# Optimization experiments

Measured on AMD Instinct MI355X. Metric: run time of the kernel, lower is better.

The kernel has to match this reference:

```python
import jax, jax.numpy as jnp
import numpy as np

DIM = 256
HEADS = 8


def _ln(x, g, b, eps=1e-5):
    mu = jnp.mean(x, axis=-1, keepdims=True)
    var = jnp.var(x, axis=-1, keepdims=True)
    return (x - mu) * jax.lax.rsqrt(var + eps) * g + b


def setup_inputs() -> dict:
    key = jax.random.key(0)
    ks = jax.random.split(key, 12)
    d = DIM
    s = lambda fan: 1.0 / np.sqrt(fan)
    return {
        "x": jax.random.normal(ks[0], (1, d, 64, 64), dtype=jnp.float32),
        "ln1_g": jnp.ones((d,), jnp.float32),
        "ln1_b": jnp.zeros((d,), jnp.float32),
        "w_qkv": jax.random.normal(ks[1], (3 * d, d), jnp.float32) * s(d),
        "b_qkv": jnp.zeros((3 * d,), jnp.float32),
        "w_proj": jax.random.normal(ks[2], (d, d), jnp.float32) * s(d),
        "b_proj": jnp.zeros((d,), jnp.float32),
        "ln2_g": jnp.ones((d,), jnp.float32),
        "ln2_b": jnp.zeros((d,), jnp.float32),
        "w_mlp1": jax.random.normal(ks[3], (4 * d, d), jnp.float32) * s(d),
        "b_mlp1": jnp.zeros((4 * d,), jnp.float32),
        "w_mlp2": jax.random.normal(ks[4], (d, 4 * d), jnp.float32) * s(4 * d),
        "b_mlp2": jnp.zeros((d,), jnp.float32),
    }


def reference(x, ln1_g, ln1_b, w_qkv, b_qkv, w_proj, b_proj,
              ln2_g, ln2_b, w_mlp1, b_mlp1, w_mlp2, b_mlp2):
    B, C, H, W = x.shape
    hd = HEADS
    d = C // hd
    scale = d ** (-0.5)
    # work channels-last: [B, H, W, C] -> [B, HW, C]
    xl = jnp.transpose(x, (0, 2, 3, 1)).reshape(B, H * W, C)

    # --- attention branch ---
    xn = _ln(xl, ln1_g, ln1_b)
    qkv = jnp.einsum('bnc,oc->bno', xn, w_qkv) + b_qkv  # [B, N, 3C]
    q, k, v = jnp.split(qkv, 3, axis=-1)
    def heads(t):  # [B,N,C] -> [B,h,N,d]
        return jnp.transpose(t.reshape(B, H * W, hd, d), (0, 2, 1, 3))
    q, k, v = heads(q), heads(k), heads(v)
    attn = jax.nn.softmax(jnp.einsum('bhnd,bhmd->bhnm', q, k) * scale, axis=-1)
    out = jnp.einsum('bhnm,bhmd->bhnd', attn, v)  # [B,h,N,d]
    out = jnp.transpose(out, (0, 2, 1, 3)).reshape(B, H * W, C)
    xl = xl + jnp.einsum('bnc,oc->bno', out, w_proj) + b_proj

    # --- MLP branch ---
    xn = _ln(xl, ln2_g, ln2_b)
    h1 = jax.nn.gelu(jnp.einsum('bnc,oc->bno', xn, w_mlp1) + b_mlp1,
                     approximate=False)
    xl = xl + jnp.einsum('bnf,of->bno', h1, w_mlp2) + b_mlp2

    return jnp.transpose(xl.reshape(B, H, W, C), (0, 3, 1, 2))
```

## Files before the change

### kernel.cpp

```cpp
#include <hip/hip_runtime.h>
#include <hip/hip_bf16.h>

typedef __bf16 bf16_t;
typedef __bf16 bf16x8 __attribute__((ext_vector_type(8)));
typedef __bf16 bf16x4 __attribute__((ext_vector_type(4)));
typedef float  f32x4  __attribute__((ext_vector_type(4)));
typedef unsigned int uint;
typedef uint u32x4 __attribute__((ext_vector_type(4)));

#define MFMA(a,b,c) __builtin_amdgcn_mfma_f32_16x16x32_bf16((a),(b),(c),0,0,0)
#define SPLIT 4

__device__ __forceinline__ size_t pidx(int n, int k, int K) {
  return (size_t)(n >> 4) * (K << 4) + ((k >> 3) << 7) + ((n & 15) << 3) + (k & 7);
}

__device__ __forceinline__ uint packbf2(float lo, float hi) {
  unsigned short a = __builtin_bit_cast(unsigned short, (bf16_t)lo);
  unsigned short b = __builtin_bit_cast(unsigned short, (bf16_t)hi);
  return (uint)a | ((uint)b << 16);
}

__global__ __launch_bounds__(256) void prep(const float* __restrict__ w_qkv,
                                            const float* __restrict__ w_proj,
                                            const float* __restrict__ w_mlp1,
                                            const float* __restrict__ w_mlp2,
                                            bf16_t* __restrict__ wq, bf16_t* __restrict__ wp,
                                            bf16_t* __restrict__ w1, bf16_t* __restrict__ w2,
                                            const float* __restrict__ x,
                                            const float* __restrict__ g,
                                            const float* __restrict__ bta,
                                            float* __restrict__ xl,
                                            bf16_t* __restrict__ xn) {
  __shared__ float tile[256][33];
  __shared__ float psum[8][32], psq[8][32], mu_s[32], rs_s[32];
  int b = blockIdx.x;
  if (b < 384) {
    const float* src; bf16_t* dst; int t0, ksh;
    if (b < 96)       { src = w_qkv;  dst = wq; ksh = 5; t0 = b * 256; }
    else if (b < 128) { src = w_proj; dst = wp; ksh = 5; t0 = (b - 96) * 256; }
    else if (b < 256) { src = w_mlp1; dst = w1; ksh = 5; t0 = (b - 128) * 256; }
    else              { src = w_mlp2; dst = w2; ksh = 7; t0 = (b - 256) * 256; }
    int t = t0 + threadIdx.x;
    int n = t >> ksh, kb = t & ((1 << ksh) - 1);
    int K = 8 << ksh;
    const float* p = src + (size_t)n * K + kb * 8;
    float4 a = *(const float4*)p;
    float4 c = *(const float4*)(p + 4);
    bf16x8 o = {(bf16_t)a.x, (bf16_t)a.y, (bf16_t)a.z, (bf16_t)a.w,
                (bf16_t)c.x, (bf16_t)c.y, (bf16_t)c.z, (bf16_t)c.w};
    *(bf16x8*)(dst + (size_t)(n >> 4) * (K << 4) + kb * 128 + ((n & 15) << 3)) = o;
    return;
  }
  int t = threadIdx.x, n0 = (b - 384) * 32;
  int lane32 = t & 31, grp = t >> 5;
#pragma unroll
  for (int it = 0; it < 32; ++it) {
    int c = grp + it * 8;
    tile[c][lane32] = x[(size_t)c * 4096 + n0 + lane32];
  }
  __syncthreads();
  float s = 0.f, sq = 0.f;
#pragma unroll
  for (int ci = 0; ci < 32; ++ci) {
    float v = tile[grp * 32 + ci][lane32];
    s += v; sq += v * v;
  }
  psum[grp][lane32] = s; psq[grp][lane32] = sq;
  __syncthreads();
  if (t < 32) {
    float S = 0.f, Q = 0.f;
#pragma unroll
    for (int p = 0; p < 8; ++p) { S += psum[p][t]; Q += psq[p][t]; }
    float mu = S * (1.0f / 256.0f);
    float var = Q * (1.0f / 256.0f) - mu * mu;
    mu_s[t] = mu; rs_s[t] = rsqrtf(var + 1e-5f);
  }
  __syncthreads();
  {
    float mu = mu_s[lane32], rs = rs_s[lane32];
    int row = n0 + lane32;
    bf16_t* op = xn + (size_t)(row >> 4) * 4096 + ((row & 15) << 3);
#pragma unroll
    for (int cc8 = 0; cc8 < 4; ++cc8) {
      int c0 = grp * 32 + cc8 * 8;
      bf16x8 o;
#pragma unroll
      for (int j = 0; j < 8; ++j) {
        int c = c0 + j;
        o[j] = (bf16_t)((tile[c][lane32] - mu) * rs * g[c] + bta[c]);
      }
      *(bf16x8*)(op + ((c0 >> 3) << 7)) = o;
    }
  }
#pragma unroll
  for (int it = 0; it < 4; ++it) {
    int j = grp + it * 8;
#pragma unroll
    for (int c0 = 0; c0 < 256; c0 += 32)
      xl[(size_t)(n0 + j) * 256 + c0 + lane32] = tile[c0 + lane32][j];
  }
}

template <int K, int EPI, int RPW, int KS = 1>
__global__ __launch_bounds__(256) void gemm_bt(const bf16_t* __restrict__ A,
                                               const bf16_t* __restrict__ W,
                                               const float* __restrict__ bias,
                                               void* __restrict__ outp, int ldn,
                                               const float* __restrict__ resid,
                                               const float* __restrict__ g2,
                                               const float* __restrict__ bt2,
                                               bf16_t* __restrict__ xn2p) {
  constexpr int RB = RPW / 16;
  constexpr int KLEN = K / KS;
  int w = threadIdx.x >> 6, lane = threadIdx.x & 63;
  int quad = lane >> 4, idx = lane & 15;
  int row0, col0;
  if constexpr (EPI == 6) { row0 = blockIdx.x * 16; col0 = w * 64; }
  else { row0 = blockIdx.x * (4 * RPW) + w * RPW; col0 = blockIdx.y * 64; }
  int kb0 = (KS > 1) ? blockIdx.z * KLEN : 0;
  f32x4 acc[RB][4];
#pragma unroll
  for (int rb = 0; rb < RB; ++rb)
#pragma unroll
    for (int nb = 0; nb < 4; ++nb) acc[rb][nb] = (f32x4){0.f, 0.f, 0.f, 0.f};
  const bf16_t* abase = A + (size_t)(row0 >> 4) * (K << 4) + quad * 128 + idx * 8;
  const bf16_t* wbase = W + (size_t)(col0 >> 4) * (K << 4) + quad * 128 + idx * 8;
#pragma unroll 4
  for (int k0 = kb0; k0 < kb0 + KLEN; k0 += 32) {
    bf16x8 a[RB];
#pragma unroll
    for (int rb = 0; rb < RB; ++rb)
      a[rb] = *(const bf16x8*)(abase + (size_t)rb * (K << 4) + k0 * 16);
#pragma unroll
    for (int nb = 0; nb < 4; ++nb) {
      bf16x8 b = *(const bf16x8*)(wbase + (size_t)nb * (K << 4) + k0 * 16);
#pragma unroll
      for (int rb = 0; rb < RB; ++rb) acc[rb][nb] = MFMA(a[rb], b, acc[rb][nb]);
    }
  }

  if constexpr (EPI == 6) {
    __shared__ float lns[4][2][16];
    __shared__ bf16_t tile[16][256];
    float vv[4][4];
    float ps[4] = {0.f, 0.f, 0.f, 0.f}, pq[4] = {0.f, 0.f, 0.f, 0.f};
#pragma unroll
    for (int nb = 0; nb < 4; ++nb) {
      int c = col0 + nb * 16 + idx;
      float bv = bias[c];
#pragma unroll
      for (int r = 0; r < 4; ++r) {
        int rr = row0 + quad * 4 + r;
        float t = acc[0][nb][r] + bv + resid[(size_t)rr * 256 + c];
        vv[nb][r] = t;
        ((float*)outp)[(size_t)rr * 256 + c] = t;
        ps[r] += t; pq[r] += t * t;
      }
    }
#pragma unroll
    for (int m = 1; m < 16; m <<= 1)
#pragma unroll
      for (int r = 0; r < 4; ++r) {
        ps[r] += __shfl_xor(ps[r], m);
        pq[r] += __shfl_xor(pq[r], m);
      }
    if (idx == 0)
#pragma unroll
      for (int r = 0; r < 4; ++r) {
        lns[w][0][quad * 4 + r] = ps[r];
        lns[w][1][quad * 4 + r] = pq[r];
      }
    __syncthreads();
    float mu[4], rs[4];
#pragma unroll
    for (int r = 0; r < 4; ++r) {
      int row = quad * 4 + r;
      float S = (lns[0][0][row] + lns[1][0][row]) + (lns[2][0][row] + lns[3][0][row]);
      float Q = (lns[0][1][row] + lns[1][1][row]) + (lns[2][1][row] + lns[3][1][row]);
      float m_ = S * (1.0f / 256.0f);
      mu[r] = m_;
      rs[r] = rsqrtf(Q * (1.0f / 256.0f) - m_ * m_ + 1e-5f);
    }
#pragma unroll
    for (int nb = 0; nb < 4; ++nb) {
      int c = col0 + nb * 16 + idx;
      float gg = g2[c], bb = bt2[c];
#pragma unroll
      for (int r = 0; r < 4; ++r)
        tile[quad * 4 + r][c] = (bf16_t)((vv[nb][r] - mu[r]) * rs[r] * gg + bb);
    }
    __syncthreads();
    {
      int t = threadIdx.x;
      int row = t >> 4, k0 = (t & 15) * 16;
      int grr = row0 + row;
      bf16_t* op = xn2p + (size_t)(grr >> 4) * 4096 + ((grr & 15) << 3);
      *(bf16x8*)(op + ((k0 >> 3) << 7)) = *(const bf16x8*)&tile[row][k0];
      *(bf16x8*)(op + (((k0 + 8) >> 3) << 7)) = *(const bf16x8*)&tile[row][k0 + 8];
    }
    return;
  }

#pragma unroll
  for (int nb = 0; nb < 4; ++nb) {
    int c = col0 + nb * 16 + idx;
    float bv = (EPI == 4) ? 0.f : bias[c];
    if constexpr (EPI == 5) {
      int n = row0 + quad * 4;
      f32x4 o;
#pragma unroll
      for (int r = 0; r < 4; ++r)
        o[r] = acc[0][nb][r] + bv + resid[(size_t)(n + r) * 256 + c];
      *(f32x4*)((float*)outp + (size_t)c * 4096 + n) = o;
    } else {
#pragma unroll
      for (int rb = 0; rb < RB; ++rb)
#pragma unroll
        for (int r = 0; r < 4; ++r) {
          int rr = row0 + rb * 16 + quad * 4 + r;
          float v = acc[rb][nb][r] + bv;
          if constexpr (EPI == 1) {
            float z = v * (0.7978845608f + 0.0356774081f * v * v);
            float t = __builtin_amdgcn_exp2f(z * 2.885390082f);
            float th = 1.f - 2.f * __builtin_amdgcn_rcpf(t + 1.f);
            v = 0.5f * v * (1.f + th);
            ((bf16_t*)outp)[pidx(rr, c, ldn)] = (bf16_t)v;
          } else if constexpr (EPI == 4) {
            ((float*)outp)[((size_t)blockIdx.z * 4096 + rr) * ldn + c] = v;
          } else {
            bf16_t* qh = (bf16_t*)outp;
            bf16_t* kh = qh + 1048576;
            bf16_t* vp = kh + 1048576;
            if (c < 256) {
              qh[(size_t)(c >> 5) * 131072 + rr * 32 + (c & 31)] = (bf16_t)v;
            } else if (c < 512) {
              kh[(size_t)((c - 256) >> 5) * 131072 + rr * 32 + (c & 31)] = (bf16_t)v;
            } else {
              vp[(size_t)((c - 512) >> 5) * 131072 + (rr >> 5) * 1024 + (c & 31) * 32 + (rr & 31)] = (bf16_t)v;
            }
          }
        }
    }
  }
}

__device__ __forceinline__ void quad_transpose(const uint p[4][2], bf16x8& lo, bf16x8& hi) {
  auto sA0 = __builtin_amdgcn_permlane32_swap((int)p[0][0], (int)p[1][0], false, false);
  auto sA1 = __builtin_amdgcn_permlane32_swap((int)p[0][1], (int)p[1][1], false, false);
  auto sB0 = __builtin_amdgcn_permlane16_swap(sA0[0], sA0[1], false, false);
  auto sB1 = __builtin_amdgcn_permlane16_swap(sA1[0], sA1[1], false, false);
  u32x4 w0 = {(uint)sB0[0], (uint)sB1[0], (uint)sB0[1], (uint)sB1[1]};
  lo = __builtin_bit_cast(bf16x8, w0);
  auto tA0 = __builtin_amdgcn_permlane32_swap((int)p[2][0], (int)p[3][0], false, false);
  auto tA1 = __builtin_amdgcn_permlane32_swap((int)p[2][1], (int)p[3][1], false, false);
  auto tB0 = __builtin_amdgcn_permlane16_swap(tA0[0], tA0[1], false, false);
  auto tB1 = __builtin_amdgcn_permlane16_swap(tA1[0], tA1[1], false, false);
  u32x4 w1 = {(uint)tB0[0], (uint)tB1[0], (uint)tB0[1], (uint)tB1[1]};
  hi = __builtin_bit_cast(bf16x8, w1);
}

__global__ __launch_bounds__(256, 4) void attn_split(const bf16_t* __restrict__ qkvh,
                                                     uint* __restrict__ o_part,
                                                     float* __restrict__ l_part) {
  int w = threadIdx.x >> 6, lane = threadIdx.x & 63;
  int quad = lane >> 4, idx = lane & 15;
  int h  = blockIdx.x & 7;
  int qt = (blockIdx.x >> 3) & 31;
  int sp = blockIdx.x >> 8;
  int qrow = qt * 128 + w * 32;
  const bf16_t* qh = qkvh + (size_t)h * 131072;
  const bf16_t* kh = qh + 8 * 131072;
  const bf16_t* vp = kh + 8 * 131072;
  const float cs = 0.25503518f;
  bf16x8 qr0 = *(const bf16x8*)(qh + (size_t)(qrow + idx) * 32 + quad * 8);
  bf16x8 qr1 = *(const bf16x8*)(qh + (size_t)(qrow + 16 + idx) * 32 + quad * 8);
  bf16x8 qf0, qf1, ones1;
#pragma unroll
  for (int j = 0; j < 8; ++j) {
    qf0[j] = (bf16_t)((float)qr0[j] * cs);
    qf1[j] = (bf16_t)((float)qr1[j] * cs);
    ones1[j] = (bf16_t)1.0f;
  }
  f32x4 o00 = {0.f,0.f,0.f,0.f}, o01 = {0.f,0.f,0.f,0.f};
  f32x4 o10 = {0.f,0.f,0.f,0.f}, o11 = {0.f,0.f,0.f,0.f};
  f32x4 lsA = {0.f,0.f,0.f,0.f}, lsB = {0.f,0.f,0.f,0.f};
  const f32x4 zero = {0.f,0.f,0.f,0.f};
  int kbase = sp * 1024;

  bf16x8 kf[4];
#pragma unroll
  for (int kb = 0; kb < 4; ++kb)
    kf[kb] = *(const bf16x8*)(kh + (size_t)(kbase + kb * 16 + idx) * 32 + quad * 8);

  for (int kt = 0; kt < 16; ++kt) {
    int k0 = kbase + kt * 64;
    int k1 = kbase + ((kt + 1) & 15) * 64;
    const bf16_t* vt = vp + (size_t)(k0 >> 5) * 1024 + quad * 8;
    bf16x8 vv0 = *(const bf16x8*)(vt + idx * 32);
    bf16x8 vv1 = *(const bf16x8*)(vt + (idx + 16) * 32);
    bf16x8 vv2 = *(const bf16x8*)(vt + 1024 + idx * 32);
    bf16x8 vv3 = *(const bf16x8*)(vt + 1024 + (idx + 16) * 32);
    bf16x8 kfn[4];
#pragma unroll
    for (int kb = 0; kb < 4; ++kb)
      kfn[kb] = *(const bf16x8*)(kh + (size_t)(k1 + kb * 16 + idx) * 32 + quad * 8);
    __builtin_amdgcn_s_setprio(1);
    uint p0[4][2], p1[4][2];
#pragma unroll
    for (int kb = 0; kb < 4; ++kb) {
      f32x4 s0 = MFMA(kf[kb], qf0, zero);
      f32x4 s1 = MFMA(kf[kb], qf1, zero);
      float a0 = __builtin_amdgcn_exp2f(s0[0]), a1 = __builtin_amdgcn_exp2f(s0[1]);
      float a2 = __builtin_amdgcn_exp2f(s0[2]), a3 = __builtin_amdgcn_exp2f(s0[3]);
      float b0 = __builtin_amdgcn_exp2f(s1[0]), b1 = __builtin_amdgcn_exp2f(s1[1]);
      float b2 = __builtin_amdgcn_exp2f(s1[2]), b3 = __builtin_amdgcn_exp2f(s1[3]);
      p0[kb][0] = packbf2(a0, a1); p0[kb][1] = packbf2(a2, a3);
      p1[kb][0] = packbf2(b0, b1); p1[kb][1] = packbf2(b2, b3);
    }
    bf16x8 pa0, pa1, pb0, pb1;
    quad_transpose(p0, pa0, pa1);
    quad_transpose(p1, pb0, pb1);
    o00 = MFMA(pa0, vv0, o00);
    o01 = MFMA(pa0, vv1, o01);
    o10 = MFMA(pb0, vv0, o10);
    o11 = MFMA(pb0, vv1, o11);
    lsA = MFMA(pa0, ones1, lsA);
    lsB = MFMA(pb0, ones1, lsB);
    o00 = MFMA(pa1, vv2, o00);
    o01 = MFMA(pa1, vv3, o01);
    o10 = MFMA(pb1, vv2, o10);
    o11 = MFMA(pb1, vv3, o11);
    lsA = MFMA(pa1, ones1, lsA);
    lsB = MFMA(pb1, ones1, lsB);
    __builtin_amdgcn_s_setprio(0);
#pragma unroll
    for (int kb = 0; kb < 4; ++kb) kf[kb] = kfn[kb];
  }
  if (idx == 0) {
    float* lp = l_part + ((size_t)sp * 8 + h) * 4096 + qrow;
#pragma unroll
    for (int r = 0; r < 4; ++r) {
      lp[quad * 4 + r]      = lsA[r];
      lp[16 + quad * 4 + r] = lsB[r];
    }
  }
#pragma unroll
  for (int r = 0; r < 4; ++r) {
    int n0 = qrow + quad * 4 + r;
    o_part[(((size_t)sp * 4096 + n0) * 8 + h) * 16 + idx] = packbf2(o00[r], o01[r]);
    int n1 = n0 + 16;
    o_part[(((size_t)sp * 4096 + n1) * 8 + h) * 16 + idx] = packbf2(o10[r], o11[r]);
  }
}

__global__ __launch_bounds__(256) void attn_norm(const uint* __restrict__ o_part,
                                                 const float* __restrict__ l_part,
                                                 bf16_t* __restrict__ attn) {
  int t = blockIdx.x * 256 + threadIdx.x;
  int j0 = (t & 3) * 4;
  int h  = (t >> 2) & 7;
  int n  = t >> 5;
  float l = 0.f;
#pragma unroll
  for (int s = 0; s < SPLIT; ++s) l += l_part[((size_t)s * 8 + h) * 4096 + n];
  float inv = 1.0f / l;
  float alo[4] = {0.f,0.f,0.f,0.f}, ahi[4] = {0.f,0.f,0.f,0.f};
#pragma unroll
  for (int s = 0; s < SPLIT; ++s) {
    const uint* p = o_part + (((size_t)s * 4096 + n) * 8 + h) * 16 + j0;
    uint4 v = *(const uint4*)p;
    uint vv[4] = {v.x, v.y, v.z, v.w};
#pragma unroll
    for (int jj = 0; jj < 4; ++jj) {
      alo[jj] += __builtin_bit_cast(float, vv[jj] << 16);
      ahi[jj] += __builtin_bit_cast(float, vv[jj] & 0xffff0000u);
    }
  }
  bf16x4 lo = {(bf16_t)(alo[0] * inv), (bf16_t)(alo[1] * inv),
               (bf16_t)(alo[2] * inv), (bf16_t)(alo[3] * inv)};
  bf16x4 hi = {(bf16_t)(ahi[0] * inv), (bf16_t)(ahi[1] * inv),
               (bf16_t)(ahi[2] * inv), (bf16_t)(ahi[3] * inv)};
  int k1 = h * 32 + j0;
  int k2 = k1 + 16;
  *(bf16x4*)(attn + (size_t)(n >> 4) * 4096 + ((k1 >> 3) << 7) + ((n & 15) << 3) + (k1 & 7)) = lo;
  *(bf16x4*)(attn + (size_t)(n >> 4) * 4096 + ((k2 >> 3) << 7) + ((n & 15) << 3) + (k2 & 7)) = hi;
}

extern "C" void kernel_launch(void* const* d_in, const int* in_sizes, int n_in,
                              void* d_out, int out_size, void* d_ws, size_t ws_size,
                              hipStream_t stream) {
  const float* x      = (const float*)d_in[0];
  const float* ln1_g  = (const float*)d_in[1];
  const float* ln1_b  = (const float*)d_in[2];
  const float* w_qkv  = (const float*)d_in[3];
  const float* b_qkv  = (const float*)d_in[4];
  const float* w_proj = (const float*)d_in[5];
  const float* b_proj = (const float*)d_in[6];
  const float* ln2_g  = (const float*)d_in[7];
  const float* ln2_b  = (const float*)d_in[8];
  const float* w_mlp1 = (const float*)d_in[9];
  const float* b_mlp1 = (const float*)d_in[10];
  const float* w_mlp2 = (const float*)d_in[11];
  const float* b_mlp2 = (const float*)d_in[12];

  char* ws = (char*)d_ws;
  bf16_t* qkvh   = (bf16_t*)(ws + 0);
  float*  xl     = (float*)(ws + (6u << 20));
  bf16_t* xn     = (bf16_t*)(ws + (10u << 20));
  uint*   o_part = (uint*)(ws + (12u << 20));
  bf16_t* attn   = (bf16_t*)(ws + (20u << 20));
  float*  xl2    = (float*)(ws + (10u << 20));
  bf16_t* xn2    = (bf16_t*)(ws + (14u << 20));
  bf16_t* h1     = (bf16_t*)(ws + 0);
  bf16_t* wq     = (bf16_t*)(ws + (32u << 20));
  bf16_t* wp     = wq + 196608;
  bf16_t* w1     = wp + 65536;
  bf16_t* w2     = w1 + 262144;
  float*  l_part = (float*)(ws + (34304u << 10));

  prep<<<512, 256, 0, stream>>>(w_qkv, w_proj, w_mlp1, w_mlp2, wq, wp, w1, w2,
                                x, ln1_g, ln1_b, xl, xn);

  gemm_bt<256, 3, 16><<<dim3(64, 12), 256, 0, stream>>>(
      xn, wq, b_qkv, qkvh, 768, nullptr, nullptr, nullptr, nullptr);
  attn_split<<<256 * SPLIT, 256, 0, stream>>>(qkvh, o_part, l_part);
  attn_norm<<<512, 256, 0, stream>>>(o_part, l_part, attn);

  gemm_bt<256, 6, 16, 1><<<256, 256, 0, stream>>>(
      attn, wp, b_proj, xl2, 256, xl, ln2_g, ln2_b, xn2);

  gemm_bt<256, 1, 16><<<dim3(64, 16), 256, 0, stream>>>(
      xn2, w1, b_mlp1, h1, 1024, nullptr, nullptr, nullptr, nullptr);
  gemm_bt<1024, 5, 16, 1><<<dim3(64, 4), 256, 0, stream>>>(
      h1, w2, b_mlp2, d_out, 256, xl2, nullptr, nullptr, nullptr);
}
```

Measured before the change: 163.8 us.

## Software-pipeline attention loop: compute next tile's P while doing current PV MFMAs

Restructures the split-K attention inner loop into a two-stage software pipeline with ping-pong K fragment buffers. The QK^T MFMAs, exp2 and transposes for tile t+1 are issued in the same block as the PV MFMAs for tile t, so the exp and transpose work can overlap with matrix work. K loads are prefetched two tiles ahead. This raises register pressure from the doubled K and P buffers, and the wrap-around loads on the last iterations fetch tiles that are never used.

```diff
diff --git a/kernel.cpp b/kernel.cpp
--- a/kernel.cpp
+++ b/kernel.cpp
@@ -287,30 +287,15 @@
   f32x4 lsA = {0.f,0.f,0.f,0.f}, lsB = {0.f,0.f,0.f,0.f};
   const f32x4 zero = {0.f,0.f,0.f,0.f};
   int kbase = sp * 1024;
-
-  bf16x8 kf[4];
-#pragma unroll
-  for (int kb = 0; kb < 4; ++kb)
-    kf[kb] = *(const bf16x8*)(kh + (size_t)(kbase + kb * 16 + idx) * 32 + quad * 8);
-
-  for (int kt = 0; kt < 16; ++kt) {
-    int k0 = kbase + kt * 64;
-    int k1 = kbase + ((kt + 1) & 15) * 64;
-    const bf16_t* vt = vp + (size_t)(k0 >> 5) * 1024 + quad * 8;
-    bf16x8 vv0 = *(const bf16x8*)(vt + idx * 32);
-    bf16x8 vv1 = *(const bf16x8*)(vt + (idx + 16) * 32);
-    bf16x8 vv2 = *(const bf16x8*)(vt + 1024 + idx * 32);
-    bf16x8 vv3 = *(const bf16x8*)(vt + 1024 + (idx + 16) * 32);
-    bf16x8 kfn[4];
-#pragma unroll
-    for (int kb = 0; kb < 4; ++kb)
-      kfn[kb] = *(const bf16x8*)(kh + (size_t)(k1 + kb * 16 + idx) * 32 + quad * 8);
-    __builtin_amdgcn_s_setprio(1);
+  const bf16_t* kfbase = kh + (size_t)idx * 32 + quad * 8;
+
+  auto make_p = [&](const bf16x8 (&kfx)[4], bf16x8& oaL, bf16x8& oaH,
+                    bf16x8& obL, bf16x8& obH) {
     uint p0[4][2], p1[4][2];
 #pragma unroll
     for (int kb = 0; kb < 4; ++kb) {
-      f32x4 s0 = MFMA(kf[kb], qf0, zero);
-      f32x4 s1 = MFMA(kf[kb], qf1, zero);
+      f32x4 s0 = MFMA(kfx[kb], qf0, zero);
+      f32x4 s1 = MFMA(kfx[kb], qf1, zero);
       float a0 = __builtin_amdgcn_exp2f(s0[0]), a1 = __builtin_amdgcn_exp2f(s0[1]);
       float a2 = __builtin_amdgcn_exp2f(s0[2]), a3 = __builtin_amdgcn_exp2f(s0[3]);
       float b0 = __builtin_amdgcn_exp2f(s1[0]), b1 = __builtin_amdgcn_exp2f(s1[1]);
@@ -318,24 +303,66 @@
       p0[kb][0] = packbf2(a0, a1); p0[kb][1] = packbf2(a2, a3);
       p1[kb][0] = packbf2(b0, b1); p1[kb][1] = packbf2(b2, b3);
     }
-    bf16x8 pa0, pa1, pb0, pb1;
-    quad_transpose(p0, pa0, pa1);
-    quad_transpose(p1, pb0, pb1);
-    o00 = MFMA(pa0, vv0, o00);
-    o01 = MFMA(pa0, vv1, o01);
-    o10 = MFMA(pb0, vv0, o10);
-    o11 = MFMA(pb0, vv1, o11);
-    lsA = MFMA(pa0, ones1, lsA);
-    lsB = MFMA(pb0, ones1, lsB);
-    o00 = MFMA(pa1, vv2, o00);
-    o01 = MFMA(pa1, vv3, o01);
-    o10 = MFMA(pb1, vv2, o10);
-    o11 = MFMA(pb1, vv3, o11);
-    lsA = MFMA(pa1, ones1, lsA);
-    lsB = MFMA(pb1, ones1, lsB);
-    __builtin_amdgcn_s_setprio(0);
-#pragma unroll
-    for (int kb = 0; kb < 4; ++kb) kf[kb] = kfn[kb];
+    quad_transpose(p0, oaL, oaH);
+    quad_transpose(p1, obL, obH);
+  };
+
+  bf16x8 kfA[4], kfB[4];
+#pragma unroll
+  for (int kb = 0; kb < 4; ++kb)
+    kfA[kb] = *(const bf16x8*)(kfbase + (size_t)(kbase + kb * 16) * 32);
+#pragma unroll
+  for (int kb = 0; kb < 4; ++kb)
+    kfB[kb] = *(const bf16x8*)(kfbase + (size_t)(kbase + 64 + kb * 16) * 32);
+
+  bf16x8 AaL, AaH, AbL, AbH;
+  bf16x8 BaL, BaH, BbL, BbH;
+  make_p(kfA, AaL, AaH, AbL, AbH);
+
+  for (int t = 0; t < 8; ++t) {
+    int kt0 = 2 * t;
+    {
+      int k0 = kbase + kt0 * 64;
+      const bf16_t* vt = vp + (size_t)(k0 >> 5) * 1024 + quad * 8;
+      bf16x8 vv0 = *(const bf16x8*)(vt + idx * 32);
+      bf16x8 vv1 = *(const bf16x8*)(vt + (idx + 16) * 32);
+      bf16x8 vv2 = *(const bf16x8*)(vt + 1024 + idx * 32);
+      bf16x8 vv3 = *(const bf16x8*)(vt + 1024 + (idx + 16) * 32);
+      int kn = kbase + ((kt0 + 2) & 15) * 64;
+#pragma unroll
+      for (int kb = 0; kb < 4; ++kb)
+        kfA[kb] = *(const bf16x8*)(kfbase + (size_t)(kn + kb * 16) * 32);
+      __builtin_amdgcn_s_setprio(1);
+      make_p(kfB, BaL, BaH, BbL, BbH);
+      o00 = MFMA(AaL, vv0, o00); o01 = MFMA(AaL, vv1, o01);
+      o10 = MFMA(AbL, vv0, o10); o11 = MFMA(AbL, vv1, o11);
+      lsA = MFMA(AaL, ones1, lsA); lsB = MFMA(AbL, ones1, lsB);
+      o00 = MFMA(AaH, vv2, o00); o01 = MFMA(AaH, vv3, o01);
+      o10 = MFMA(AbH, vv2, o10); o11 = MFMA(AbH, vv3, o11);
+      lsA = MFMA(AaH, ones1, lsA); lsB = MFMA(AbH, ones1, lsB);
+      __builtin_amdgcn_s_setprio(0);
+    }
+    {
+      int k0 = kbase + (kt0 + 1) * 64;
+      const bf16_t* vt = vp + (size_t)(k0 >> 5) * 1024 + quad * 8;
+      bf16x8 vv0 = *(const bf16x8*)(vt + idx * 32);
+      bf16x8 vv1 = *(const bf16x8*)(vt + (idx + 16) * 32);
+      bf16x8 vv2 = *(const bf16x8*)(vt + 1024 + idx * 32);
+      bf16x8 vv3 = *(const bf16x8*)(vt + 1024 + (idx + 16) * 32);
+      int kn = kbase + ((kt0 + 3) & 15) * 64;
+#pragma unroll
+      for (int kb = 0; kb < 4; ++kb)
+        kfB[kb] = *(const bf16x8*)(kfbase + (size_t)(kn + kb * 16) * 32);
+      __builtin_amdgcn_s_setprio(1);
+      make_p(kfA, AaL, AaH, AbL, AbH);
+      o00 = MFMA(BaL, vv0, o00); o01 = MFMA(BaL, vv1, o01);
+      o10 = MFMA(BbL, vv0, o10); o11 = MFMA(BbL, vv1, o11);
+      lsA = MFMA(BaL, ones1, lsA); lsB = MFMA(BbL, ones1, lsB);
+      o00 = MFMA(BaH, vv2, o00); o01 = MFMA(BaH, vv3, o01);
+      o10 = MFMA(BbH, vv2, o10); o11 = MFMA(BbH, vv3, o11);
+      lsA = MFMA(BaH, ones1, lsA); lsB = MFMA(BbH, ones1, lsB);
+      __builtin_amdgcn_s_setprio(0);
+    }
   }
   if (idx == 0) {
     float* lp = l_part + ((size_t)sp * 8 + h) * 4096 + qrow;
```

After: 173.1 us. 5.6% more time.

## Fuse split-K attention reduction into attention kernel via shared memory

Applied to the files above, without the earlier changes.

Each block now covers 32 query rows of one head, and its four waves each handle a different quarter of the keys instead of separate blocks per split. The partial outputs and row sums are combined in shared memory and normalised in the same kernel, which removes the attn_norm launch and the global round trip of bf16 partials. In exchange, every wave of a block now reads a different range of K/V, so K/V reuse across waves within a block is lost, and a block barrier plus extra LDS traffic is added. The partials also stay in fp32 rather than being rounded to bf16 before the reduction.

```diff
diff --git a/kernel.cpp b/kernel.cpp
--- a/kernel.cpp
+++ b/kernel.cpp
@@ -9,7 +9,6 @@
 typedef uint u32x4 __attribute__((ext_vector_type(4)));
 
 #define MFMA(a,b,c) __builtin_amdgcn_mfma_f32_16x16x32_bf16((a),(b),(c),0,0,0)
-#define SPLIT 4
 
 __device__ __forceinline__ size_t pidx(int n, int k, int K) {
   return (size_t)(n >> 4) * (K << 4) + ((k >> 3) << 7) + ((n & 15) << 3) + (k & 7);
@@ -260,15 +259,15 @@
   hi = __builtin_bit_cast(bf16x8, w1);
 }
 
-__global__ __launch_bounds__(256, 4) void attn_split(const bf16_t* __restrict__ qkvh,
-                                                     uint* __restrict__ o_part,
-                                                     float* __restrict__ l_part) {
+__global__ __launch_bounds__(256, 4) void attn_fused(const bf16_t* __restrict__ qkvh,
+                                                     bf16_t* __restrict__ attn) {
+  __shared__ float sO[4][32][33];
+  __shared__ float sL[4][32];
   int w = threadIdx.x >> 6, lane = threadIdx.x & 63;
   int quad = lane >> 4, idx = lane & 15;
   int h  = blockIdx.x & 7;
-  int qt = (blockIdx.x >> 3) & 31;
-  int sp = blockIdx.x >> 8;
-  int qrow = qt * 128 + w * 32;
+  int qt = blockIdx.x >> 3;
+  int qrow = qt * 32;
   const bf16_t* qh = qkvh + (size_t)h * 131072;
   const bf16_t* kh = qh + 8 * 131072;
   const bf16_t* vp = kh + 8 * 131072;
@@ -286,7 +285,7 @@
   f32x4 o10 = {0.f,0.f,0.f,0.f}, o11 = {0.f,0.f,0.f,0.f};
   f32x4 lsA = {0.f,0.f,0.f,0.f}, lsB = {0.f,0.f,0.f,0.f};
   const f32x4 zero = {0.f,0.f,0.f,0.f};
-  int kbase = sp * 1024;
+  int kbase = w * 1024;
 
   bf16x8 kf[4];
 #pragma unroll
@@ -337,54 +336,40 @@
 #pragma unroll
     for (int kb = 0; kb < 4; ++kb) kf[kb] = kfn[kb];
   }
+#pragma unroll
+  for (int r = 0; r < 4; ++r) {
+    int rl = quad * 4 + r;
+    sO[w][rl][idx]           = o00[r];
+    sO[w][rl][idx + 16]      = o01[r];
+    sO[w][16 + rl][idx]      = o10[r];
+    sO[w][16 + rl][idx + 16] = o11[r];
+  }
   if (idx == 0) {
-    float* lp = l_part + ((size_t)sp * 8 + h) * 4096 + qrow;
 #pragma unroll
     for (int r = 0; r < 4; ++r) {
-      lp[quad * 4 + r]      = lsA[r];
-      lp[16 + quad * 4 + r] = lsB[r];
-    }
-  }
-#pragma unroll
-  for (int r = 0; r < 4; ++r) {
-    int n0 = qrow + quad * 4 + r;
-    o_part[(((size_t)sp * 4096 + n0) * 8 + h) * 16 + idx] = packbf2(o00[r], o01[r]);
-    int n1 = n0 + 16;
-    o_part[(((size_t)sp * 4096 + n1) * 8 + h) * 16 + idx] = packbf2(o10[r], o11[r]);
-  }
-}
-
-__global__ __launch_bounds__(256) void attn_norm(const uint* __restrict__ o_part,
-                                                 const float* __restrict__ l_part,
-                                                 bf16_t* __restrict__ attn) {
-  int t = blockIdx.x * 256 + threadIdx.x;
-  int j0 = (t & 3) * 4;
-  int h  = (t >> 2) & 7;
-  int n  = t >> 5;
-  float l = 0.f;
-#pragma unroll
-  for (int s = 0; s < SPLIT; ++s) l += l_part[((size_t)s * 8 + h) * 4096 + n];
-  float inv = 1.0f / l;
-  float alo[4] = {0.f,0.f,0.f,0.f}, ahi[4] = {0.f,0.f,0.f,0.f};
-#pragma unroll
-  for (int s = 0; s < SPLIT; ++s) {
-    const uint* p = o_part + (((size_t)s * 4096 + n) * 8 + h) * 16 + j0;
-    uint4 v = *(const uint4*)p;
-    uint vv[4] = {v.x, v.y, v.z, v.w};
-#pragma unroll
-    for (int jj = 0; jj < 4; ++jj) {
-      alo[jj] += __builtin_bit_cast(float, vv[jj] << 16);
-      ahi[jj] += __builtin_bit_cast(float, vv[jj] & 0xffff0000u);
-    }
-  }
-  bf16x4 lo = {(bf16_t)(alo[0] * inv), (bf16_t)(alo[1] * inv),
-               (bf16_t)(alo[2] * inv), (bf16_t)(alo[3] * inv)};
-  bf16x4 hi = {(bf16_t)(ahi[0] * inv), (bf16_t)(ahi[1] * inv),
-               (bf16_t)(ahi[2] * inv), (bf16_t)(ahi[3] * inv)};
-  int k1 = h * 32 + j0;
-  int k2 = k1 + 16;
-  *(bf16x4*)(attn + (size_t)(n >> 4) * 4096 + ((k1 >> 3) << 7) + ((n & 15) << 3) + (k1 & 7)) = lo;
-  *(bf16x4*)(attn + (size_t)(n >> 4) * 4096 + ((k2 >> 3) << 7) + ((n & 15) << 3) + (k2 & 7)) = hi;
+      sL[w][quad * 4 + r]      = lsA[r];
+      sL[w][16 + quad * 4 + r] = lsB[r];
+    }
+  }
+  __syncthreads();
+  {
+    int t = threadIdx.x;
+    int row = t >> 3, d0 = (t & 7) * 4;
+    float l = (sL[0][row] + sL[1][row]) + (sL[2][row] + sL[3][row]);
+    float inv = 1.0f / l;
+    float v[4];
+#pragma unroll
+    for (int j = 0; j < 4; ++j) {
+      int d = d0 + j;
+      v[j] = (sO[0][row][d] + sO[1][row][d]) + (sO[2][row][d] + sO[3][row][d]);
+    }
+    bf16x4 o = {(bf16_t)(v[0] * inv), (bf16_t)(v[1] * inv),
+                (bf16_t)(v[2] * inv), (bf16_t)(v[3] * inv)};
+    int n = qrow + row;
+    int k = h * 32 + d0;
+    *(bf16x4*)(attn + (size_t)(n >> 4) * 4096 + ((k >> 3) << 7) +
+               ((n & 15) << 3) + (k & 7)) = o;
+  }
 }
 
 extern "C" void kernel_launch(void* const* d_in, const int* in_sizes, int n_in,
@@ -408,7 +393,6 @@
   bf16_t* qkvh   = (bf16_t*)(ws + 0);
   float*  xl     = (float*)(ws + (6u << 20));
   bf16_t* xn     = (bf16_t*)(ws + (10u << 20));
-  uint*   o_part = (uint*)(ws + (12u << 20));
   bf16_t* attn   = (bf16_t*)(ws + (20u << 20));
   float*  xl2    = (float*)(ws + (10u << 20));
   bf16_t* xn2    = (bf16_t*)(ws + (14u << 20));
@@ -417,15 +401,13 @@
   bf16_t* wp     = wq + 196608;
   bf16_t* w1     = wp + 65536;
   bf16_t* w2     = w1 + 262144;
-  float*  l_part = (float*)(ws + (34304u << 10));
 
   prep<<<512, 256, 0, stream>>>(w_qkv, w_proj, w_mlp1, w_mlp2, wq, wp, w1, w2,
                                 x, ln1_g, ln1_b, xl, xn);
 
   gemm_bt<256, 3, 16><<<dim3(64, 12), 256, 0, stream>>>(
       xn, wq, b_qkv, qkvh, 768, nullptr, nullptr, nullptr, nullptr);
-  attn_split<<<256 * SPLIT, 256, 0, stream>>>(qkvh, o_part, l_part);
-  attn_norm<<<512, 256, 0, stream>>>(o_part, l_part, attn);
+  attn_fused<<<1024, 256, 0, stream>>>(qkvh, attn);
 
   gemm_bt<256, 6, 16, 1><<<256, 256, 0, stream>>>(
       attn, wp, b_proj, xl2, 256, xl, ln2_g, ln2_b, xn2);
```

Result: faster. 159.0 us (-2.9%).
